# Kernel optimization log

Hardware: AMD Instinct MI355X
Metric: run time of the kernel (lower is better)

The kernel has to match this reference:

```python
import jax, jax.numpy as jnp
import numpy as np

DIM = 1024
HEADS = 16
DIM_HEAD = 64
INNER = HEADS * DIM_HEAD
SEQ = 4096
BATCH = 1


def setup_inputs() -> dict:
    key = jax.random.key(0)
    ks = jax.random.split(key, 6)
    s = 0.02
    return {
        "x": jax.random.normal(ks[0], (BATCH, SEQ, DIM), dtype=jnp.float32),
        "Wq": jax.random.normal(ks[1], (DIM, INNER), dtype=jnp.float32) * s,
        "Wk": jax.random.normal(ks[2], (DIM, INNER), dtype=jnp.float32) * s,
        "Wv": jax.random.normal(ks[3], (DIM, INNER), dtype=jnp.float32) * s,
        "Wo": jax.random.normal(ks[4], (INNER, DIM), dtype=jnp.float32) * s,
        "bo": jax.random.normal(ks[5], (DIM,), dtype=jnp.float32) * s,
    }


def reference(x, Wq, Wk, Wv, Wo, bo):
    b, n, _ = x.shape
    beta = 1.0 / jnp.sqrt(jnp.float32(DIM_HEAD))
    # project and split heads: [b, n, inner] -> [b, h, n, d]
    def split_heads(t):
        return t.reshape(b, n, HEADS, DIM_HEAD).transpose(0, 2, 1, 3)
    q = split_heads(x @ Wq)
    k = split_heads(x @ Wk)
    v = split_heads(x @ Wv)
    # scaled scores [b, h, n, n]
    scores = jnp.einsum('bhid,bhjd->bhij', q * beta, k)
    mask_value = -jnp.finfo(scores.dtype).max
    causal = jnp.triu(jnp.ones((n, n), dtype=bool), k=1)
    scores = jnp.where(causal, mask_value, scores)
    attn = jax.nn.softmax(scores, axis=-1)
    out = jnp.einsum('bhij,bhjd->bhid', attn, v)
    out = out.transpose(0, 2, 1, 3).reshape(b, n, INNER)
    # output projection (dropout is identity in eval)
    return out @ Wo + bo
```

## Files before the change

kernel.cpp:

```cpp
#include <hip/hip_runtime.h>
#include <hip/hip_bf16.h>
#include <stdint.h>
#include <math.h>

#define SEQ 4096
#define DIM 1024
#define NHEADS 16
#define DHEAD 64
#define INNER 1024

typedef __hip_bfloat16 bf16;
typedef __attribute__((ext_vector_type(8))) short short8;
typedef __attribute__((ext_vector_type(4))) float floatx4;
typedef __attribute__((ext_vector_type(16))) float floatx16;

__device__ __forceinline__ void gll16(const bf16* g, bf16* l) {
    __builtin_amdgcn_global_load_lds(
        (const __attribute__((address_space(1))) unsigned int*)g,
        (__attribute__((address_space(3))) unsigned int*)l,
        16, 0, 0);
}

__device__ __forceinline__ unsigned short f2bf_bits(float f) {
    bf16 h = __float2bfloat16(f);
    return *reinterpret_cast<unsigned short*>(&h);
}

__device__ __forceinline__ uint2 pack4bf(float a, float b, float c, float d) {
    __hip_bfloat162 lo = __float22bfloat162_rn(float2{a, b});
    __hip_bfloat162 hi = __float22bfloat162_rn(float2{c, d});
    uint2 r;
    r.x = *reinterpret_cast<unsigned*>(&lo);
    r.y = *reinterpret_cast<unsigned*>(&hi);
    return r;
}

__device__ __forceinline__ unsigned pkbf(float lo, float hi) {
    __hip_bfloat162 h = __float22bfloat162_rn(float2{lo, hi});
    return *reinterpret_cast<unsigned*>(&h);
}

__global__ __launch_bounds__(256) void prep_kernel(
        const float* __restrict__ x, const float* __restrict__ W0,
        const float* __restrict__ W1, const float* __restrict__ W2,
        const float* __restrict__ W3, bf16* __restrict__ xb,
        bf16* __restrict__ T0, bf16* __restrict__ T1,
        bf16* __restrict__ T2, bf16* __restrict__ T3) {
    const int tid = threadIdx.x + threadIdx.y * blockDim.x;
    if (blockIdx.z == 4) {
        int chunk = blockIdx.y * 32 + blockIdx.x;
        int base = chunk * 4096 + tid * 4;
        #pragma unroll
        for (int r = 0; r < 4; r++) {
            int i = base + r * 1024;
            float4 f = *reinterpret_cast<const float4*>(x + i);
            unsigned long long p = (unsigned long long)f2bf_bits(f.x)
                                 | ((unsigned long long)f2bf_bits(f.y) << 16)
                                 | ((unsigned long long)f2bf_bits(f.z) << 32)
                                 | ((unsigned long long)f2bf_bits(f.w) << 48);
            *reinterpret_cast<unsigned long long*>(xb + i) = p;
        }
        return;
    }
    const float* W; bf16* T;
    switch (blockIdx.z) {
        case 0:  W = W0; T = T0; break;
        case 1:  W = W1; T = T1; break;
        case 2:  W = W2; T = T2; break;
        default: W = W3; T = T3; break;
    }
    __shared__ float tile[32][33];
    int k0 = blockIdx.x * 32, n0 = blockIdx.y * 32;
    int tx = threadIdx.x, ty = threadIdx.y;
    #pragma unroll
    for (int i = 0; i < 4; i++)
        tile[ty + 8 * i][tx] = W[(size_t)(k0 + ty + 8 * i) * 1024 + n0 + tx];
    __syncthreads();
    #pragma unroll
    for (int i = 0; i < 4; i++)
        T[(size_t)(n0 + ty + 8 * i) * 1024 + k0 + tx] = __float2bfloat16(tile[tx][ty + 8 * i]);
}

__device__ __forceinline__ void gemm128_dbuf(const bf16* __restrict__ A,
                                             const bf16* __restrict__ Bt,
                                             int m0, int n0, floatx4 acc[4][4]) {
    __shared__ __align__(16) bf16 As[2][8192];
    __shared__ __align__(16) bf16 Bs[2][8192];
    const int tid = threadIdx.x;
    const int wave = tid >> 6;
    const int lane = tid & 63;
    const int l15 = lane & 15;
    const int quad = lane >> 4;

    #pragma unroll
    for (int i = 0; i < 4; i++)
        #pragma unroll
        for (int j = 0; j < 4; j++)
            acc[i][j] = (floatx4){0.f, 0.f, 0.f, 0.f};

    auto stage = [&](int buf, int k0) {
        #pragma unroll
        for (int j = 0; j < 4; j++) {
            int t = wave * 4 + j;
            int row = (t >> 1) * 16 + l15;
            int kb = (t & 1) * 32 + quad * 8;
            gll16(A + (size_t)(m0 + row) * 1024 + k0 + kb, &As[buf][t * 512]);
            gll16(Bt + (size_t)(n0 + row) * 1024 + k0 + kb, &Bs[buf][t * 512]);
        }
    };

    stage(0, 0);
    __syncthreads();
    int cur = 0;
    for (int k0 = 0; k0 < 1024; k0 += 64) {
        if (k0 + 64 < 1024) stage(cur ^ 1, k0 + 64);
        #pragma unroll
        for (int ks = 0; ks < 2; ks++) {
            short8 af[4], bfr[4];
            #pragma unroll
            for (int i = 0; i < 4; i++)
                af[i] = *reinterpret_cast<const short8*>(
                    &As[cur][((((wave >> 1) * 4 + i) * 2 + ks) * 512) + lane * 8]);
            #pragma unroll
            for (int j = 0; j < 4; j++)
                bfr[j] = *reinterpret_cast<const short8*>(
                    &Bs[cur][((((wave & 1) * 4 + j) * 2 + ks) * 512) + lane * 8]);
            #pragma unroll
            for (int i = 0; i < 4; i++)
                #pragma unroll
                for (int j = 0; j < 4; j++)
                    acc[i][j] = __builtin_amdgcn_mfma_f32_16x16x32_bf16(af[i], bfr[j], acc[i][j], 0, 0, 0);
        }
        __syncthreads();
        cur ^= 1;
    }
}

__global__ __launch_bounds__(512, 2) void qkv_gemm_kernel(
        const bf16* __restrict__ xb,
        const bf16* __restrict__ Wqt, const bf16* __restrict__ Wkt, const bf16* __restrict__ Wvt,
        bf16* __restrict__ Qh, bf16* __restrict__ Kh, bf16* __restrict__ Vt) {
    __shared__ __align__(16) bf16 As[2][16384];
    __shared__ __align__(16) bf16 Bs[2][16384];
    const bf16* Bt;
    if (blockIdx.z == 0)      Bt = Wqt;
    else if (blockIdx.z == 1) Bt = Wkt;
    else                      Bt = Wvt;
    const int n0 = blockIdx.x * 256, m0 = blockIdx.y * 256;
    const int tid = threadIdx.x;
    const int wave = tid >> 6;
    const int lane = tid & 63;
    const int l15 = lane & 15, quad = lane >> 4;
    const int wr = wave >> 2;
    const int wc = wave & 3;

    floatx4 acc[8][4];
    #pragma unroll
    for (int i = 0; i < 8; i++)
        #pragma unroll
        for (int j = 0; j < 4; j++)
            acc[i][j] = (floatx4){0.f, 0.f, 0.f, 0.f};

    auto stage = [&](int buf, int k0) {
        #pragma unroll
        for (int j = 0; j < 4; j++) {
            int t = wave * 4 + j;
            int row = (t >> 1) * 16 + l15;
            int kb = (t & 1) * 32 + quad * 8;
            gll16(xb + (size_t)(m0 + row) * 1024 + k0 + kb, &As[buf][t * 512]);
            gll16(Bt + (size_t)(n0 + row) * 1024 + k0 + kb, &Bs[buf][t * 512]);
        }
    };

    stage(0, 0);
    __syncthreads();
    int cur = 0;
    for (int k0 = 0; k0 < 1024; k0 += 64) {
        if (k0 + 64 < 1024) stage(cur ^ 1, k0 + 64);
        #pragma unroll
        for (int ks = 0; ks < 2; ks++) {
            short8 af[8], bfr[4];
            #pragma unroll
            for (int i = 0; i < 8; i++)
                af[i] = *reinterpret_cast<const short8*>(
                    &As[cur][(((wr * 8 + i) * 2 + ks) * 512) + lane * 8]);
            #pragma unroll
            for (int j = 0; j < 4; j++)
                bfr[j] = *reinterpret_cast<const short8*>(
                    &Bs[cur][(((wc * 4 + j) * 2 + ks) * 512) + lane * 8]);
            #pragma unroll
            for (int i = 0; i < 8; i++)
                #pragma unroll
                for (int j = 0; j < 4; j++)
                    acc[i][j] = __builtin_amdgcn_mfma_f32_16x16x32_bf16(af[i], bfr[j], acc[i][j], 0, 0, 0);
        }
        __syncthreads();
        cur ^= 1;
    }

    const int wm = wr * 128, wn = wc * 64;
    if (blockIdx.z == 2) {
        #pragma unroll
        for (int i = 0; i < 8; i++)
            #pragma unroll
            for (int j = 0; j < 4; j++) {
                int col = n0 + wn + j * 16 + l15;
                int h = col >> 6, d = col & 63;
                int row0 = m0 + wm + i * 16 + quad * 4;
                uint2 v = pack4bf(acc[i][j][0], acc[i][j][1], acc[i][j][2], acc[i][j][3]);
                *reinterpret_cast<uint2*>(Vt + ((size_t)h * DHEAD + d) * SEQ + row0) = v;
            }
    } else {
        bf16* O = (blockIdx.z == 0) ? Qh : Kh;
        float scale = (blockIdx.z == 0) ? 0.125f * 1.4426950408889634f : 1.0f;
        #pragma unroll
        for (int i = 0; i < 8; i++)
            #pragma unroll
            for (int j = 0; j < 4; j++) {
                int col = n0 + wn + j * 16 + l15;
                int h = col >> 6, d = col & 63;
                #pragma unroll
                for (int r = 0; r < 4; r++) {
                    int row = m0 + wm + i * 16 + quad * 4 + r;
                    O[((size_t)h * SEQ + row) * DHEAD + d] = __float2bfloat16(acc[i][j][r] * scale);
                }
            }
    }
}

__global__ __launch_bounds__(256, 2) void out_gemm_kernel(
        const bf16* __restrict__ Oa, const bf16* __restrict__ Wot,
        const float* __restrict__ bo, float* __restrict__ out) {
    int n0 = blockIdx.x * 128, m0 = blockIdx.y * 128;
    floatx4 acc[4][4];
    gemm128_dbuf(Oa, Wot, m0, n0, acc);

    const int tid = threadIdx.x, wave = tid >> 6, lane = tid & 63;
    const int l15 = lane & 15, quad = lane >> 4;
    const int wm = (wave >> 1) * 64, wn = (wave & 1) * 64;
    #pragma unroll
    for (int i = 0; i < 4; i++)
        #pragma unroll
        for (int j = 0; j < 4; j++) {
            int col = n0 + wn + j * 16 + l15;
            float b = bo[col];
            #pragma unroll
            for (int r = 0; r < 4; r++) {
                int row = m0 + wm + i * 16 + quad * 4 + r;
                out[(size_t)row * DIM + col] = acc[i][j][r] + b;
            }
        }
}

#define PV_STEP(P, KTG)                                                              \
    do {                                                                             \
        const int rb_ = ((KTG) & 1) * 8;                                             \
        unsigned A0_ = pkbf((P)[rb_ + 0], (P)[rb_ + 1]);                             \
        unsigned B0_ = pkbf((P)[rb_ + 4], (P)[rb_ + 5]);                             \
        unsigned A1_ = pkbf((P)[rb_ + 2], (P)[rb_ + 3]);                             \
        unsigned B1_ = pkbf((P)[rb_ + 6], (P)[rb_ + 7]);                             \
        asm("v_permlane32_swap_b32 %0, %1" : "+v"(A0_), "+v"(B0_));                  \
        asm("v_permlane32_swap_b32 %0, %1" : "+v"(A1_), "+v"(B1_));                  \
        uint4 w_; w_.x = A0_; w_.y = A1_; w_.z = B0_; w_.w = B1_;                    \
        short8 bp_ = *reinterpret_cast<short8*>(&w_);                                \
        short8 av0_ = *reinterpret_cast<const short8*>(                              \
            &Vsh[cur][(KTG) * 512 + lane * 8]);                                      \
        short8 av1_ = *reinterpret_cast<const short8*>(                              \
            &Vsh[cur][(4 + (KTG)) * 512 + lane * 8]);                                \
        acc0 = __builtin_amdgcn_mfma_f32_32x32x16_bf16(av0_, bp_, acc0, 0, 0, 0);    \
        acc1 = __builtin_amdgcn_mfma_f32_32x32x16_bf16(av1_, bp_, acc1, 0, 0, 0);    \
    } while (0)

__global__ __launch_bounds__(256, 4) void attention_kernel(
        const bf16* __restrict__ Qh, const bf16* __restrict__ Kh,
        const bf16* __restrict__ Vt, bf16* __restrict__ Oa,
        float* __restrict__ Op0, float* __restrict__ Op1,
        float* __restrict__ L0, float* __restrict__ L1) {
    __shared__ __align__(16) bf16 Ksh[2][4096];
    __shared__ __align__(16) bf16 Vsh[2][4096];
    const int tid = threadIdx.x, wave = tid >> 6, lane = tid & 63;
    const int ql = lane & 31, half = lane >> 5;
    const int h8 = half * 8;
    const int id = blockIdx.x;
    const int head = id & 15;
    const int rk = id >> 4;
    int t, ck;
    if (rk < 16)      { t = 16 + rk; ck = 0; }
    else if (rk < 32) { t = 47 - rk; ck = 1; }
    else              { t = rk - 32; ck = 0; }
    const bool split = (t >= 16);
    const int ktile0 = (split && ck == 1) ? 32 : 0;
    const int ktile1 = (split && ck == 0) ? 32 : (2 * t + 2);
    const int qw = t * 128 + wave * 32;
    const int q = qw + ql;
    const size_t hoff = (size_t)head * SEQ * DHEAD;
    const bf16* Qb = Qh + hoff;
    const bf16* Kb = Kh + hoff;
    const bf16* Vb = Vt + hoff;

    short8 bq[4];
    #pragma unroll
    for (int kc = 0; kc < 4; kc++)
        bq[kc] = *reinterpret_cast<const short8*>(
            Qb + (size_t)q * DHEAD + kc * 16 + h8);

    floatx16 acc0, acc1;
    #pragma unroll
    for (int r = 0; r < 16; r++) { acc0[r] = 0.f; acc1[r] = 0.f; }
    float l_part = 0.f;

    auto stage = [&](int buf, int kbase) {
        #pragma unroll
        for (int j = 0; j < 2; j++) {
            int tc = wave * 2 + j;
            gll16(Kb + (size_t)(kbase + (tc >> 2) * 32 + ql) * DHEAD + (tc & 3) * 16 + h8,
                  &Ksh[buf][tc * 512]);
            gll16(Vb + (size_t)((tc >> 2) * 32 + ql) * SEQ + kbase + (tc & 3) * 16 + h8,
                  &Vsh[buf][tc * 512]);
        }
    };

    stage(0, ktile0 * 64);
    __syncthreads();
    int cur = 0;
    for (int kt = ktile0; kt < ktile1; kt++) {
        const int kbase = kt * 64;
        if (kt + 1 < ktile1) stage(cur ^ 1, (kt + 1) * 64);

        floatx16 s0, s1;
        #pragma unroll
        for (int r = 0; r < 16; r++) { s0[r] = 0.f; s1[r] = 0.f; }
        __builtin_amdgcn_s_setprio(1);
        #pragma unroll
        for (int kc = 0; kc < 4; kc++) {
            short8 ak0 = *reinterpret_cast<const short8*>(&Ksh[cur][kc * 512 + lane * 8]);
            short8 ak1 = *reinterpret_cast<const short8*>(&Ksh[cur][(4 + kc) * 512 + lane * 8]);
            s0 = __builtin_amdgcn_mfma_f32_32x32x16_bf16(ak0, bq[kc], s0, 0, 0, 0);
            s1 = __builtin_amdgcn_mfma_f32_32x32x16_bf16(ak1, bq[kc], s1, 0, 0, 0);
        }
        __builtin_amdgcn_s_setprio(0);
        if (kbase + 63 > qw) {
            int base0 = kbase + half * 4 - q;
            #pragma unroll
            for (int r = 0; r < 16; r++) {
                int off = (r & 3) + 8 * (r >> 2);
                if (base0 + off > 0)      s0[r] = -1e30f;
                if (base0 + 32 + off > 0) s1[r] = -1e30f;
            }
        }
        #pragma unroll
        for (int r = 0; r < 16; r++) {
            s0[r] = __builtin_amdgcn_exp2f(s0[r]);
            s1[r] = __builtin_amdgcn_exp2f(s1[r]);
            l_part += s0[r] + s1[r];
        }
        __builtin_amdgcn_s_setprio(1);
        PV_STEP(s0, 0); PV_STEP(s0, 1); PV_STEP(s1, 2); PV_STEP(s1, 3);
        __builtin_amdgcn_s_setprio(0);

        __syncthreads();
        cur ^= 1;
    }
    float l = l_part + __shfl_xor(l_part, 32, 64);
    if (!split) {
        float rcp = 1.0f / l;
        #pragma unroll
        for (int a = 0; a < 4; a++) {
            int d0 = 8 * a + half * 4;
            uint2 v0 = pack4bf(acc0[4 * a + 0] * rcp, acc0[4 * a + 1] * rcp,
                               acc0[4 * a + 2] * rcp, acc0[4 * a + 3] * rcp);
            *reinterpret_cast<uint2*>(Oa + (size_t)q * INNER + head * DHEAD + d0) = v0;
            uint2 v1 = pack4bf(acc1[4 * a + 0] * rcp, acc1[4 * a + 1] * rcp,
                               acc1[4 * a + 2] * rcp, acc1[4 * a + 3] * rcp);
            *reinterpret_cast<uint2*>(Oa + (size_t)q * INNER + head * DHEAD + 32 + d0) = v1;
        }
    } else {
        float* Op = ck ? Op1 : Op0;
        float* Lp = ck ? L1 : L0;
        if (half == 0) Lp[head * 2048 + (q - 2048)] = l;
        #pragma unroll
        for (int a = 0; a < 4; a++) {
            int d0 = 8 * a + half * 4;
            floatx4 v0 = {acc0[4 * a + 0], acc0[4 * a + 1], acc0[4 * a + 2], acc0[4 * a + 3]};
            *reinterpret_cast<floatx4*>(
                Op + (size_t)(q - 2048) * INNER + head * DHEAD + d0) = v0;
            floatx4 v1 = {acc1[4 * a + 0], acc1[4 * a + 1], acc1[4 * a + 2], acc1[4 * a + 3]};
            *reinterpret_cast<floatx4*>(
                Op + (size_t)(q - 2048) * INNER + head * DHEAD + 32 + d0) = v1;
        }
    }
}

__global__ __launch_bounds__(256) void combine_kernel(
        const float* __restrict__ Op0, const float* __restrict__ Op1,
        const float* __restrict__ L0, const float* __restrict__ L1,
        bf16* __restrict__ Oa) {
    int idx = blockIdx.x * 256 + threadIdx.x;
    int row = idx >> 8;
    int c4 = (idx & 255) * 4;
    int head = c4 >> 6;
    float l = L0[head * 2048 + row] + L1[head * 2048 + row];
    float rcp = 1.0f / l;
    float4 a = *reinterpret_cast<const float4*>(Op0 + (size_t)row * INNER + c4);
    float4 b = *reinterpret_cast<const float4*>(Op1 + (size_t)row * INNER + c4);
    uint2 v = pack4bf((a.x + b.x) * rcp, (a.y + b.y) * rcp,
                      (a.z + b.z) * rcp, (a.w + b.w) * rcp);
    *reinterpret_cast<uint2*>(Oa + (size_t)(2048 + row) * INNER + c4) = v;
}

extern "C" void kernel_launch(void* const* d_in, const int* in_sizes, int n_in,
                              void* d_out, int out_size, void* d_ws, size_t ws_size,
                              hipStream_t stream) {
    const float* x  = (const float*)d_in[0];
    const float* Wq = (const float*)d_in[1];
    const float* Wk = (const float*)d_in[2];
    const float* Wv = (const float*)d_in[3];
    const float* Wo = (const float*)d_in[4];
    const float* bo = (const float*)d_in[5];
    float* out = (float*)d_out;

    char* ws = (char*)d_ws;
    size_t off = 0;
    bf16* xb  = (bf16*)(ws + off); off += (size_t)SEQ * DIM * 2;
    bf16* Wqt = (bf16*)(ws + off); off += (size_t)DIM * INNER * 2;
    bf16* Wkt = (bf16*)(ws + off); off += (size_t)DIM * INNER * 2;
    bf16* Wvt = (bf16*)(ws + off); off += (size_t)DIM * INNER * 2;
    bf16* Wot = (bf16*)(ws + off); off += (size_t)INNER * DIM * 2;
    bf16* Qh  = (bf16*)(ws + off); off += (size_t)NHEADS * SEQ * DHEAD * 2;
    bf16* Kh  = (bf16*)(ws + off); off += (size_t)NHEADS * SEQ * DHEAD * 2;
    bf16* Vtr = (bf16*)(ws + off); off += (size_t)NHEADS * DHEAD * SEQ * 2;
    bf16* Oa  = (bf16*)(ws + off); off += (size_t)SEQ * INNER * 2;
    float* Op0 = (float*)(ws + off); off += (size_t)(SEQ / 2) * INNER * 4;
    float* Op1 = (float*)(ws + off); off += (size_t)(SEQ / 2) * INNER * 4;
    float* L0  = (float*)(ws + off); off += (size_t)NHEADS * (SEQ / 2) * 4;
    float* L1  = (float*)(ws + off); off += (size_t)NHEADS * (SEQ / 2) * 4;

    prep_kernel<<<dim3(32, 32, 5), dim3(32, 8), 0, stream>>>(x, Wq, Wk, Wv, Wo,
                                                             xb, Wqt, Wkt, Wvt, Wot);
    qkv_gemm_kernel<<<dim3(4, 16, 3), 512, 0, stream>>>(xb, Wqt, Wkt, Wvt, Qh, Kh, Vtr);
    attention_kernel<<<768, 256, 0, stream>>>(Qh, Kh, Vtr, Oa, Op0, Op1, L0, L1);
    combine_kernel<<<2048, 256, 0, stream>>>(Op0, Op1, L0, L1, Oa);
    out_gemm_kernel<<<dim3(8, 32), 256, 0, stream>>>(Oa, Wot, bo, out);
}
```

Measured before the change: 225.5 us.

## Split causal attention KV range into up to three chunks for load balance

Changes the attention work split. Long query tiles (t 22-31) are now split into three KV chunks and medium tiles (t 11-21) into two, replacing the previous two-way split of the upper half only. The grid grows from 768 to 1008 blocks so that per-block work is more even across CUs. The cost is more fp32 partial outputs to write and a combine pass covering 2688 rows, with a third partial buffer for some of them.

Measured after the change: 232.6 us. +3.1%, slower.

```diff
diff --git a/kernel.cpp b/kernel.cpp
--- a/kernel.cpp
+++ b/kernel.cpp
@@ -274,8 +274,8 @@
 __global__ __launch_bounds__(256, 4) void attention_kernel(
         const bf16* __restrict__ Qh, const bf16* __restrict__ Kh,
         const bf16* __restrict__ Vt, bf16* __restrict__ Oa,
-        float* __restrict__ Op0, float* __restrict__ Op1,
-        float* __restrict__ L0, float* __restrict__ L1) {
+        float* __restrict__ Op0, float* __restrict__ Op1, float* __restrict__ Op2,
+        float* __restrict__ L0, float* __restrict__ L1, float* __restrict__ L2) {
     __shared__ __align__(16) bf16 Ksh[2][4096];
     __shared__ __align__(16) bf16 Vsh[2][4096];
     const int tid = threadIdx.x, wave = tid >> 6, lane = tid & 63;
@@ -283,14 +283,16 @@
     const int h8 = half * 8;
     const int id = blockIdx.x;
     const int head = id & 15;
-    const int rk = id >> 4;
-    int t, ck;
-    if (rk < 16)      { t = 16 + rk; ck = 0; }
-    else if (rk < 32) { t = 47 - rk; ck = 1; }
-    else              { t = rk - 32; ck = 0; }
-    const bool split = (t >= 16);
-    const int ktile0 = (split && ck == 1) ? 32 : 0;
-    const int ktile1 = (split && ck == 0) ? 32 : (2 * t + 2);
+    const int pk = id >> 4;
+    int t, j, n;
+    if (pk < 30)      { t = 31 - pk / 3;            j = pk % 3;  n = 3; }
+    else if (pk < 52) { int q2 = pk - 30; t = 21 - (q2 >> 1); j = q2 & 1; n = 2; }
+    else              { t = 62 - pk;                j = 0;       n = 1; }
+    const int len = 2 * t + 2;
+    const int base = len / n, rem = len % n;
+    const int plen = base + (j < rem ? 1 : 0);
+    const int pstart = j * base + (j < rem ? j : rem);
+    const int ktile0 = pstart, ktile1 = pstart + plen;
     const int qw = t * 128 + wave * 32;
     const int q = qw + ql;
     const size_t hoff = (size_t)head * SEQ * DHEAD;
@@ -311,8 +313,8 @@
 
     auto stage = [&](int buf, int kbase) {
         #pragma unroll
-        for (int j = 0; j < 2; j++) {
-            int tc = wave * 2 + j;
+        for (int jj = 0; jj < 2; jj++) {
+            int tc = wave * 2 + jj;
             gll16(Kb + (size_t)(kbase + (tc >> 2) * 32 + ql) * DHEAD + (tc & 3) * 16 + h8,
                   &Ksh[buf][tc * 512]);
             gll16(Vb + (size_t)((tc >> 2) * 32 + ql) * SEQ + kbase + (tc & 3) * 16 + h8,
@@ -362,7 +364,7 @@
         cur ^= 1;
     }
     float l = l_part + __shfl_xor(l_part, 32, 64);
-    if (!split) {
+    if (n == 1) {
         float rcp = 1.0f / l;
         #pragma unroll
         for (int a = 0; a < 4; a++) {
@@ -375,37 +377,44 @@
             *reinterpret_cast<uint2*>(Oa + (size_t)q * INNER + head * DHEAD + 32 + d0) = v1;
         }
     } else {
-        float* Op = ck ? Op1 : Op0;
-        float* Lp = ck ? L1 : L0;
-        if (half == 0) Lp[head * 2048 + (q - 2048)] = l;
+        float* Op = (j == 0) ? Op0 : (j == 1) ? Op1 : Op2;
+        float* Lp = (j == 0) ? L0 : (j == 1) ? L1 : L2;
+        const int rowoff = q - 1408;
+        if (half == 0) Lp[head * 2688 + rowoff] = l;
         #pragma unroll
         for (int a = 0; a < 4; a++) {
             int d0 = 8 * a + half * 4;
             floatx4 v0 = {acc0[4 * a + 0], acc0[4 * a + 1], acc0[4 * a + 2], acc0[4 * a + 3]};
             *reinterpret_cast<floatx4*>(
-                Op + (size_t)(q - 2048) * INNER + head * DHEAD + d0) = v0;
+                Op + (size_t)rowoff * INNER + head * DHEAD + d0) = v0;
             floatx4 v1 = {acc1[4 * a + 0], acc1[4 * a + 1], acc1[4 * a + 2], acc1[4 * a + 3]};
             *reinterpret_cast<floatx4*>(
-                Op + (size_t)(q - 2048) * INNER + head * DHEAD + 32 + d0) = v1;
+                Op + (size_t)rowoff * INNER + head * DHEAD + 32 + d0) = v1;
         }
     }
 }
 
 __global__ __launch_bounds__(256) void combine_kernel(
         const float* __restrict__ Op0, const float* __restrict__ Op1,
+        const float* __restrict__ Op2,
         const float* __restrict__ L0, const float* __restrict__ L1,
-        bf16* __restrict__ Oa) {
-    int idx = blockIdx.x * 256 + threadIdx.x;
-    int row = idx >> 8;
-    int c4 = (idx & 255) * 4;
-    int head = c4 >> 6;
-    float l = L0[head * 2048 + row] + L1[head * 2048 + row];
+        const float* __restrict__ L2, bf16* __restrict__ Oa) {
+    const int rowoff = blockIdx.x;
+    const int c4 = threadIdx.x * 4;
+    const int t = (1408 + rowoff) >> 7;
+    const int n = (t >= 22) ? 3 : 2;
+    const int head = c4 >> 6;
+    const int li = head * 2688 + rowoff;
+    float l = L0[li] + L1[li] + (n == 3 ? L2[li] : 0.f);
     float rcp = 1.0f / l;
-    float4 a = *reinterpret_cast<const float4*>(Op0 + (size_t)row * INNER + c4);
-    float4 b = *reinterpret_cast<const float4*>(Op1 + (size_t)row * INNER + c4);
-    uint2 v = pack4bf((a.x + b.x) * rcp, (a.y + b.y) * rcp,
-                      (a.z + b.z) * rcp, (a.w + b.w) * rcp);
-    *reinterpret_cast<uint2*>(Oa + (size_t)(2048 + row) * INNER + c4) = v;
+    const size_t ro = (size_t)rowoff * INNER + c4;
+    float4 a = *reinterpret_cast<const float4*>(Op0 + ro);
+    float4 b = *reinterpret_cast<const float4*>(Op1 + ro);
+    float4 c = {0.f, 0.f, 0.f, 0.f};
+    if (n == 3) c = *reinterpret_cast<const float4*>(Op2 + ro);
+    uint2 v = pack4bf((a.x + b.x + c.x) * rcp, (a.y + b.y + c.y) * rcp,
+                      (a.z + b.z + c.z) * rcp, (a.w + b.w + c.w) * rcp);
+    *reinterpret_cast<uint2*>(Oa + (size_t)(1408 + rowoff) * INNER + c4) = v;
 }
 
 extern "C" void kernel_launch(void* const* d_in, const int* in_sizes, int n_in,
@@ -430,15 +439,17 @@
     bf16* Kh  = (bf16*)(ws + off); off += (size_t)NHEADS * SEQ * DHEAD * 2;
     bf16* Vtr = (bf16*)(ws + off); off += (size_t)NHEADS * DHEAD * SEQ * 2;
     bf16* Oa  = (bf16*)(ws + off); off += (size_t)SEQ * INNER * 2;
-    float* Op0 = (float*)(ws + off); off += (size_t)(SEQ / 2) * INNER * 4;
-    float* Op1 = (float*)(ws + off); off += (size_t)(SEQ / 2) * INNER * 4;
-    float* L0  = (float*)(ws + off); off += (size_t)NHEADS * (SEQ / 2) * 4;
-    float* L1  = (float*)(ws + off); off += (size_t)NHEADS * (SEQ / 2) * 4;
+    float* Op0 = (float*)(ws + off); off += (size_t)2688 * INNER * 4;
+    float* Op1 = (float*)(ws + off); off += (size_t)2688 * INNER * 4;
+    float* Op2 = (float*)(ws + off); off += (size_t)2688 * INNER * 4;
+    float* L0  = (float*)(ws + off); off += (size_t)NHEADS * 2688 * 4;
+    float* L1  = (float*)(ws + off); off += (size_t)NHEADS * 2688 * 4;
+    float* L2  = (float*)(ws + off); off += (size_t)NHEADS * 2688 * 4;
 
     prep_kernel<<<dim3(32, 32, 5), dim3(32, 8), 0, stream>>>(x, Wq, Wk, Wv, Wo,
                                                              xb, Wqt, Wkt, Wvt, Wot);
     qkv_gemm_kernel<<<dim3(4, 16, 3), 512, 0, stream>>>(xb, Wqt, Wkt, Wvt, Qh, Kh, Vtr);
-    attention_kernel<<<768, 256, 0, stream>>>(Qh, Kh, Vtr, Oa, Op0, Op1, L0, L1);
-    combine_kernel<<<2048, 256, 0, stream>>>(Op0, Op1, L0, L1, Oa);
+    attention_kernel<<<1008, 256, 0, stream>>>(Qh, Kh, Vtr, Oa, Op0, Op1, Op2, L0, L1, L2);
+    combine_kernel<<<2688, 256, 0, stream>>>(Op0, Op1, Op2, L0, L1, L2, Oa);
     out_gemm_kernel<<<dim3(8, 32), 256, 0, stream>>>(Oa, Wot, bo, out);
 }
```
